# Kernel tuning notes

Measured on AMD Instinct MI355X. Metric: run time of the kernel, lower is better.

The kernel has to match this reference:

```python
import jax, jax.numpy as jnp
import numpy as np

LN_EPS = 1e-5  # torch nn.LayerNorm default


def _layernorm(h):
    # elementwise_affine=False LayerNorm over last dim
    mu = jnp.mean(h, axis=-1, keepdims=True)
    var = jnp.var(h, axis=-1, keepdims=True)
    return (h - mu) * jax.lax.rsqrt(var + LN_EPS)


def setup_inputs() -> dict:
    key = jax.random.key(0)
    ks = jax.random.split(key, 7)
    B, M, D, L = 10240, 8, 512, 3  # b=1024*10 and m=8 are hardcoded in the module
    rn = lambda k, shape, scale=1.0: jax.random.normal(k, shape, dtype=jnp.float32) * scale
    return {
        "x":   rn(ks[0], (B, D)),
        "Ws":  rn(ks[1], (L, M, D, D), 0.05),  # per-layer basis weight tensors (m,i,j)
        "bs":  rn(ks[2], (L, M, D), 0.05),     # per-layer basis biases (m,i)
        "pWs": rn(ks[3], (L, B, M)),           # per-sample weight-mixing coeffs
        "pbs": rn(ks[4], (L, B, M)),           # per-sample bias-mixing coeffs
        "gWs": rn(ks[5], (L, B, D, 1)),        # gates (squeezed in forward)
        "gbs": rn(ks[6], (L, B, D)),
    }


def reference(x, Ws, bs, pWs, pbs, gWs, gbs):
    L = Ws.shape[0]
    for l in range(L):
        gW = gWs[l][..., 0]                                  # (b, i)
        # 'bi,bm,mij,bj->bi' without materializing (b,i,j):
        y = jnp.einsum('mij,bj->bmi', Ws[l], x)              # (b, m, i)
        Wx = gW * jnp.einsum('bm,bmi->bi', pWs[l], y)        # (b, i)
        # 'bj,bm,mj->bj' (bias lives in output dim)
        bias = gbs[l] * jnp.einsum('bm,mi->bi', pbs[l], bs[l])
        h = Wx + bias
        if l != L - 1:  # hidden layers: LayerNorm (no affine) + ELU; last: identity
            h = jax.nn.elu(_layernorm(h))
        x = h
    return x
```

## Files before the change

kernel.cpp:

```cpp
#include <hip/hip_runtime.h>
#include <math.h>

#define BB   10240
#define DD   512
#define MM   8

typedef _Float16 h8 __attribute__((ext_vector_type(8)));
typedef float    f4 __attribute__((ext_vector_type(4)));

__device__ __forceinline__ void gload16(const void* g, void* l) {
    __builtin_amdgcn_global_load_lds(
        (__attribute__((address_space(1))) void*)(g),
        (__attribute__((address_space(3))) void*)(l), 16, 0, 0);
}

__global__ void __launch_bounds__(256) cvt_f32_f16(const float* __restrict__ s,
                                                   _Float16* __restrict__ d, int n8) {
    int i = blockIdx.x * 256 + threadIdx.x;
    if (i >= n8) return;
    const float4* sp = (const float4*)s + (size_t)i * 2;
    float4 a = sp[0], b = sp[1];
    h8 o = { (_Float16)a.x, (_Float16)a.y, (_Float16)a.z, (_Float16)a.w,
             (_Float16)b.x, (_Float16)b.y, (_Float16)b.z, (_Float16)b.w };
    *(h8*)(d + (size_t)i * 8) = o;
}

template <int HALF_OUT>
__global__ void __launch_bounds__(128, 2) gemm_layer(
    const _Float16* __restrict__ xh,
    const _Float16* __restrict__ Wh,
    const float*  __restrict__ pW,
    const float*  __restrict__ pb,
    const float*  __restrict__ bsv,
    const float*  __restrict__ gW,
    const float*  __restrict__ gb,
    float* __restrict__ outf,
    _Float16* __restrict__ outh)
{
    __shared__ __align__(16) _Float16 Wl[2][3][32 * 64];
    __shared__ __align__(16) _Float16 Ab[128 * 64];

    const int tid  = threadIdx.x;
    const int lane = tid & 63;
    const int w    = tid >> 6;
    const int ln16 = lane & 15, quad = lane >> 4;
    const int bn0  = blockIdx.x * 64;
    const int bm0  = blockIdx.y * 128;

    _Float16 pwh[8][8];
    #pragma unroll
    for (int mt = 0; mt < 8; ++mt) {
        const float* pp = pW + (size_t)(bm0 + mt * 16 + ln16) * MM;
        float4 p0 = *(const float4*)pp;
        float4 p1 = *(const float4*)(pp + 4);
        pwh[mt][0] = (_Float16)p0.x; pwh[mt][1] = (_Float16)p0.y;
        pwh[mt][2] = (_Float16)p0.z; pwh[mt][3] = (_Float16)p0.w;
        pwh[mt][4] = (_Float16)p1.x; pwh[mt][5] = (_Float16)p1.y;
        pwh[mt][6] = (_Float16)p1.z; pwh[mt][7] = (_Float16)p1.w;
    }

    f4 acc[8][2] = {};
    h8 afr[2][8];

#define STW(S_, M_, JC_) do {                                                  \
    _Pragma("unroll")                                                          \
    for (int c = 0; c < 4; ++c) {                                              \
        int rit     = c * 8 + (lane >> 3);                                     \
        int logical = (lane & 7) ^ (lane >> 3);                                \
        const _Float16* gp = Wh + (size_t)(M_) * (DD * DD)                     \
                               + (size_t)(bn0 + w * 32 + rit) * DD             \
                               + (JC_) * 64 + logical * 8;                     \
        gload16(gp, &Wl[w][S_][c * 512]);                                      \
    }                                                                          \
} while (0)

#define STA(JC_) do {                                                          \
    _Pragma("unroll")                                                          \
    for (int c = 0; c < 8; ++c) {                                              \
        int rit     = w * 64 + c * 8 + (lane >> 3);                            \
        int logical = (lane & 7) ^ (lane >> 3);                                \
        const _Float16* gp = xh + (size_t)(bm0 + rit) * DD                     \
                                + (JC_) * 64 + logical * 8;                    \
        gload16(gp, &Ab[rit * 64]);                                            \
    }                                                                          \
} while (0)

#define AFR() do {                                                             \
    _Pragma("unroll")                                                          \
    for (int _ks = 0; _ks < 2; ++_ks)                                          \
        _Pragma("unroll")                                                      \
        for (int _mt = 0; _mt < 8; ++_mt) {                                    \
            int _phys = (_ks * 4 + quad) ^ (ln16 & 7);                         \
            afr[_ks][_mt] = *(const h8*)&Ab[(_mt * 16 + ln16) * 64             \
                                            + _phys * 8];                      \
        }                                                                      \
} while (0)

#define GS(T_, N_, AF_, SA_, B1_, B2_) do {                                    \
    if ((T_) + 2 <= 63) STW((((T_) + 2) % 3), (((T_) + 2) & 7),                \
                            (((T_) + 2) >> 3));                                \
    asm volatile("s_waitcnt vmcnt(%0)" :: "i"(N_) : "memory");                 \
    __builtin_amdgcn_sched_barrier(0);                                         \
    if (AF_) AFR();                                                            \
    h8 wfr[2][2];                                                              \
    _Pragma("unroll")                                                          \
    for (int ks = 0; ks < 2; ++ks)                                             \
        _Pragma("unroll")                                                      \
        for (int nt = 0; nt < 2; ++nt) {                                       \
            int row  = nt * 16 + ln16;                                         \
            int phys = (ks * 4 + quad) ^ (ln16 & 7);                           \
            wfr[ks][nt] = *(const h8*)&Wl[w][(T_) % 3][row * 64 + phys * 8];   \
        }                                                                      \
    _Pragma("unroll")                                                          \
    for (int ks = 0; ks < 2; ++ks)                                             \
        _Pragma("unroll")                                                      \
        for (int mt = 0; mt < 8; ++mt) {                                       \
            h8 as = afr[ks][mt] * pwh[mt][(T_) & 7];      \
            acc[mt][0] = __builtin_amdgcn_mfma_f32_16x16x32_f16(               \
                as, wfr[ks][0], acc[mt][0], 0, 0, 0);                          \
            acc[mt][1] = __builtin_amdgcn_mfma_f32_16x16x32_f16(               \
                as, wfr[ks][1], acc[mt][1], 0, 0, 0);                          \
        }                                                                      \
    if (SA_) STA(((T_) >> 3) + 1);                                             \
    if (B2_) { asm volatile("s_waitcnt lgkmcnt(0)" ::: "memory");              \
               __builtin_amdgcn_s_barrier();                                   \
               asm volatile("" ::: "memory"); }                                \
    if (B1_) { __builtin_amdgcn_s_barrier();                                   \
               asm volatile("" ::: "memory"); }                                \
} while (0)

    STA(0);
    STW(0, 0, 0);
    STW(1, 1, 0);
    asm volatile("s_waitcnt vmcnt(8)" ::: "memory");
    __builtin_amdgcn_sched_barrier(0);
    __builtin_amdgcn_s_barrier();
    asm volatile("" ::: "memory");

    GS(  0,  8, 1, 0, 0, 1);
    GS(  1,  8, 0, 0, 0, 0);
    GS(  2,  8, 0, 1, 0, 0);
    GS(  3, 16, 0, 0, 0, 0);
    GS(  4, 16, 0, 0, 0, 0);
    GS(  5,  8, 0, 0, 0, 0);
    GS(  6,  8, 0, 0, 0, 0);
    GS(  7,  8, 0, 0, 1, 0);
    GS(  8,  8, 1, 0, 0, 1);
    GS(  9,  8, 0, 0, 0, 0);
    GS( 10,  8, 0, 1, 0, 0);
    GS( 11, 16, 0, 0, 0, 0);
    GS( 12, 16, 0, 0, 0, 0);
    GS( 13,  8, 0, 0, 0, 0);
    GS( 14,  8, 0, 0, 0, 0);
    GS( 15,  8, 0, 0, 1, 0);
    GS( 16,  8, 1, 0, 0, 1);
    GS( 17,  8, 0, 0, 0, 0);
    GS( 18,  8, 0, 1, 0, 0);
    GS( 19, 16, 0, 0, 0, 0);
    GS( 20, 16, 0, 0, 0, 0);
    GS( 21,  8, 0, 0, 0, 0);
    GS( 22,  8, 0, 0, 0, 0);
    GS( 23,  8, 0, 0, 1, 0);
    GS( 24,  8, 1, 0, 0, 1);
    GS( 25,  8, 0, 0, 0, 0);
    GS( 26,  8, 0, 1, 0, 0);
    GS( 27, 16, 0, 0, 0, 0);
    GS( 28, 16, 0, 0, 0, 0);
    GS( 29,  8, 0, 0, 0, 0);
    GS( 30,  8, 0, 0, 0, 0);
    GS( 31,  8, 0, 0, 1, 0);
    GS( 32,  8, 1, 0, 0, 1);
    GS( 33,  8, 0, 0, 0, 0);
    GS( 34,  8, 0, 1, 0, 0);
    GS( 35, 16, 0, 0, 0, 0);
    GS( 36, 16, 0, 0, 0, 0);
    GS( 37,  8, 0, 0, 0, 0);
    GS( 38,  8, 0, 0, 0, 0);
    GS( 39,  8, 0, 0, 1, 0);
    GS( 40,  8, 1, 0, 0, 1);
    GS( 41,  8, 0, 0, 0, 0);
    GS( 42,  8, 0, 1, 0, 0);
    GS( 43, 16, 0, 0, 0, 0);
    GS( 44, 16, 0, 0, 0, 0);
    GS( 45,  8, 0, 0, 0, 0);
    GS( 46,  8, 0, 0, 0, 0);
    GS( 47,  8, 0, 0, 1, 0);
    GS( 48,  8, 1, 0, 0, 1);
    GS( 49,  8, 0, 0, 0, 0);
    GS( 50,  8, 0, 1, 0, 0);
    GS( 51, 16, 0, 0, 0, 0);
    GS( 52, 16, 0, 0, 0, 0);
    GS( 53,  8, 0, 0, 0, 0);
    GS( 54,  8, 0, 0, 0, 0);
    GS( 55,  8, 0, 0, 1, 0);
    GS( 56,  8, 1, 0, 0, 0);
    GS( 57,  8, 0, 0, 0, 0);
    GS( 58,  8, 0, 0, 0, 0);
    GS( 59,  8, 0, 0, 0, 0);
    GS( 60,  8, 0, 0, 0, 0);
    GS( 61,  8, 0, 0, 0, 0);
    GS( 62,  4, 0, 0, 0, 0);
    GS( 63,  0, 0, 0, 0, 0);

#undef GS
#undef AFR
#undef STA
#undef STW

    const int i0 = bn0 + w * 32 + ln16;
    const int i1 = i0 + 16;
    float bs0[8], bs1[8];
    #pragma unroll
    for (int m2 = 0; m2 < 8; ++m2) {
        bs0[m2] = bsv[m2 * DD + i0];
        bs1[m2] = bsv[m2 * DD + i1];
    }
    #pragma unroll
    for (int mt = 0; mt < 8; ++mt) {
        #pragma unroll
        for (int r = 0; r < 4; ++r) {
            int b = bm0 + mt * 16 + quad * 4 + r;
            float4 p0 = *(const float4*)(pb + (size_t)b * MM);
            float4 p1 = *(const float4*)(pb + (size_t)b * MM + 4);
            float bias0 = p0.x*bs0[0] + p0.y*bs0[1] + p0.z*bs0[2] + p0.w*bs0[3]
                        + p1.x*bs0[4] + p1.y*bs0[5] + p1.z*bs0[6] + p1.w*bs0[7];
            float bias1 = p0.x*bs1[0] + p0.y*bs1[1] + p0.z*bs1[2] + p0.w*bs1[3]
                        + p1.x*bs1[4] + p1.y*bs1[5] + p1.z*bs1[6] + p1.w*bs1[7];
            float v0 = gW[(size_t)b * DD + i0] * acc[mt][0][r] + gb[(size_t)b * DD + i0] * bias0;
            float v1 = gW[(size_t)b * DD + i1] * acc[mt][1][r] + gb[(size_t)b * DD + i1] * bias1;
            if (HALF_OUT) {
                outh[(size_t)b * DD + i0] = (_Float16)v0;
                outh[(size_t)b * DD + i1] = (_Float16)v1;
            } else {
                outf[(size_t)b * DD + i0] = v0;
                outf[(size_t)b * DD + i1] = v1;
            }
        }
    }
}

__global__ void __launch_bounds__(256) ln_elu_h(const _Float16* __restrict__ h,
                                                _Float16* __restrict__ xo) {
    const int w    = threadIdx.x >> 6;
    const int lane = threadIdx.x & 63;
    const int row  = blockIdx.x * 4 + w;
    h8 v = *(const h8*)(h + (size_t)row * DD + lane * 8);
    float f[8], s = 0.f, q = 0.f;
    #pragma unroll
    for (int i = 0; i < 8; ++i) { f[i] = (float)v[i]; s += f[i]; q += f[i] * f[i]; }
    #pragma unroll
    for (int off = 1; off < 64; off <<= 1) {
        s += __shfl_xor(s, off);
        q += __shfl_xor(q, off);
    }
    float mu   = s * (1.0f / 512.0f);
    float var  = q * (1.0f / 512.0f) - mu * mu;
    float rstd = rsqrtf(var + 1e-5f);
    h8 o;
    #pragma unroll
    for (int i = 0; i < 8; ++i) {
        float t = (f[i] - mu) * rstd;
        t = t > 0.0f ? t : expm1f(t);
        o[i] = (_Float16)t;
    }
    *(h8*)(xo + (size_t)row * DD + lane * 8) = o;
}

extern "C" void kernel_launch(void* const* d_in, const int* in_sizes, int n_in,
                              void* d_out, int out_size, void* d_ws, size_t ws_size,
                              hipStream_t stream) {
    const float* x   = (const float*)d_in[0];
    const float* Ws  = (const float*)d_in[1];
    const float* bs  = (const float*)d_in[2];
    const float* pWs = (const float*)d_in[3];
    const float* pbs = (const float*)d_in[4];
    const float* gWs = (const float*)d_in[5];
    const float* gbs = (const float*)d_in[6];
    float* out = (float*)d_out;

    _Float16* Wh = (_Float16*)d_ws;
    _Float16* xh = Wh + (size_t)3 * MM * DD * DD;
    _Float16* hh = xh + (size_t)BB * DD;

    const int wsl = MM * DD * DD;
    const int bsl = MM * DD;
    const int pl  = BB * MM;
    const int gl  = BB * DD;

    cvt_f32_f16<<<3072, 256, 0, stream>>>(Ws, Wh, 786432);
    cvt_f32_f16<<<2560, 256, 0, stream>>>(x, xh, 655360);

    dim3 gg(DD / 64, BB / 128);

    gemm_layer<1><<<gg, 128, 0, stream>>>(xh, Wh, pWs, pbs, bs, gWs, gbs,
                                          nullptr, hh);
    ln_elu_h<<<BB / 4, 256, 0, stream>>>(hh, xh);
    gemm_layer<1><<<gg, 128, 0, stream>>>(xh, Wh + wsl, pWs + pl, pbs + pl,
                                          bs + bsl, gWs + gl, gbs + gl,
                                          nullptr, hh);
    ln_elu_h<<<BB / 4, 256, 0, stream>>>(hh, xh);
    gemm_layer<0><<<gg, 128, 0, stream>>>(xh, Wh + 2 * wsl, pWs + 2 * pl,
                                          pbs + 2 * pl, bs + 2 * bsl,
                                          gWs + 2 * gl, gbs + 2 * gl,
                                          out, nullptr);
}
```

Before: 361.2 us.

## Shrink GEMM tile to 64 rows, deepen W pipeline, prefetch B fragments, fuse converts

Halves the batch tile of the layer GEMM from 128 to 64 rows, doubling the grid and raising launch bounds to 3 blocks per CU. The weight staging ring goes from 3 to 4 stages, and LDS-to-register weight fragments are double-buffered one step ahead. The A-tile load is issued earlier in each step. The two fp32-to-fp16 conversion kernels are merged into one launch. Each B tile is reused across fewer rows, so more weight traffic per FLOP is traded for better occupancy and latency hiding.

```diff
diff --git a/kernel.cpp b/kernel.cpp
--- a/kernel.cpp
+++ b/kernel.cpp
@@ -14,19 +14,26 @@
         (__attribute__((address_space(3))) void*)(l), 16, 0, 0);
 }
 
-__global__ void __launch_bounds__(256) cvt_f32_f16(const float* __restrict__ s,
-                                                   _Float16* __restrict__ d, int n8) {
+#define N8_WS 786432
+#define N8_X  655360
+__global__ void __launch_bounds__(256) cvt_all(const float* __restrict__ Ws,
+                                               const float* __restrict__ x,
+                                               _Float16* __restrict__ Wh,
+                                               _Float16* __restrict__ xh) {
     int i = blockIdx.x * 256 + threadIdx.x;
-    if (i >= n8) return;
-    const float4* sp = (const float4*)s + (size_t)i * 2;
+    const float* s; _Float16* d; int idx;
+    if (i < N8_WS)            { s = Ws; d = Wh; idx = i; }
+    else if (i < N8_WS + N8_X){ s = x;  d = xh; idx = i - N8_WS; }
+    else return;
+    const float4* sp = (const float4*)s + (size_t)idx * 2;
     float4 a = sp[0], b = sp[1];
     h8 o = { (_Float16)a.x, (_Float16)a.y, (_Float16)a.z, (_Float16)a.w,
              (_Float16)b.x, (_Float16)b.y, (_Float16)b.z, (_Float16)b.w };
-    *(h8*)(d + (size_t)i * 8) = o;
+    *(h8*)(d + (size_t)idx * 8) = o;
 }
 
 template <int HALF_OUT>
-__global__ void __launch_bounds__(128, 2) gemm_layer(
+__global__ void __launch_bounds__(128, 3) gemm_layer(
     const _Float16* __restrict__ xh,
     const _Float16* __restrict__ Wh,
     const float*  __restrict__ pW,
@@ -37,19 +44,19 @@
     float* __restrict__ outf,
     _Float16* __restrict__ outh)
 {
-    __shared__ __align__(16) _Float16 Wl[2][3][32 * 64];
-    __shared__ __align__(16) _Float16 Ab[128 * 64];
+    __shared__ __align__(16) _Float16 Wl[2][4][32 * 64];
+    __shared__ __align__(16) _Float16 Ab[64 * 64];
 
     const int tid  = threadIdx.x;
     const int lane = tid & 63;
     const int w    = tid >> 6;
     const int ln16 = lane & 15, quad = lane >> 4;
     const int bn0  = blockIdx.x * 64;
-    const int bm0  = blockIdx.y * 128;
-
-    _Float16 pwh[8][8];
-    #pragma unroll
-    for (int mt = 0; mt < 8; ++mt) {
+    const int bm0  = blockIdx.y * 64;
+
+    _Float16 pwh[4][8];
+    #pragma unroll
+    for (int mt = 0; mt < 4; ++mt) {
         const float* pp = pW + (size_t)(bm0 + mt * 16 + ln16) * MM;
         float4 p0 = *(const float4*)pp;
         float4 p1 = *(const float4*)(pp + 4);
@@ -59,8 +66,9 @@
         pwh[mt][6] = (_Float16)p1.z; pwh[mt][7] = (_Float16)p1.w;
     }
 
-    f4 acc[8][2] = {};
-    h8 afr[2][8];
+    f4 acc[4][2] = {};
+    h8 afr[2][4];
+    h8 wfr[2][2][2];
 
 #define STW(S_, M_, JC_) do {                                                  \
     _Pragma("unroll")                                                          \
@@ -76,12 +84,12 @@
 
 #define STA(JC_) do {                                                          \
     _Pragma("unroll")                                                          \
-    for (int c = 0; c < 8; ++c) {                                              \
-        int rit     = w * 64 + c * 8 + (lane >> 3);                            \
+    for (int c = 0; c < 4; ++c) {                                              \
+        int rit     = w * 32 + c * 8 + (lane >> 3);                            \
         int logical = (lane & 7) ^ (lane >> 3);                                \
         const _Float16* gp = xh + (size_t)(bm0 + rit) * DD                     \
                                 + (JC_) * 64 + logical * 8;                    \
-        gload16(gp, &Ab[rit * 64]);                                            \
+        gload16(gp, &Ab[(w * 32 + c * 8) * 64]);                               \
     }                                                                          \
 } while (0)
 
@@ -89,7 +97,7 @@
     _Pragma("unroll")                                                          \
     for (int _ks = 0; _ks < 2; ++_ks)                                          \
         _Pragma("unroll")                                                      \
-        for (int _mt = 0; _mt < 8; ++_mt) {                                    \
+        for (int _mt = 0; _mt < 4; ++_mt) {                                    \
             int _phys = (_ks * 4 + quad) ^ (ln16 & 7);                         \
             afr[_ks][_mt] = *(const h8*)&Ab[(_mt * 16 + ln16) * 64             \
                                             + _phys * 8];                      \
@@ -97,31 +105,33 @@
 } while (0)
 
 #define GS(T_, N_, AF_, SA_, B1_, B2_) do {                                    \
-    if ((T_) + 2 <= 63) STW((((T_) + 2) % 3), (((T_) + 2) & 7),                \
-                            (((T_) + 2) >> 3));                                \
+    if ((T_) + 3 <= 63) STW((((T_) + 3) & 3), (((T_) + 3) & 7),                \
+                            (((T_) + 3) >> 3));                                \
+    if (SA_) STA(((T_) >> 3) + 1);                                             \
     asm volatile("s_waitcnt vmcnt(%0)" :: "i"(N_) : "memory");                 \
     __builtin_amdgcn_sched_barrier(0);                                         \
     if (AF_) AFR();                                                            \
-    h8 wfr[2][2];                                                              \
+    if ((T_) < 63) {                                                           \
+        _Pragma("unroll")                                                      \
+        for (int ks = 0; ks < 2; ++ks)                                         \
+            _Pragma("unroll")                                                  \
+            for (int nt = 0; nt < 2; ++nt) {                                   \
+                int row  = nt * 16 + ln16;                                     \
+                int phys = (ks * 4 + quad) ^ (ln16 & 7);                       \
+                wfr[((T_) + 1) & 1][ks][nt] =                                  \
+                    *(const h8*)&Wl[w][((T_) + 1) & 3][row * 64 + phys * 8];   \
+            }                                                                  \
+    }                                                                          \
     _Pragma("unroll")                                                          \
     for (int ks = 0; ks < 2; ++ks)                                             \
         _Pragma("unroll")                                                      \
-        for (int nt = 0; nt < 2; ++nt) {                                       \
-            int row  = nt * 16 + ln16;                                         \
-            int phys = (ks * 4 + quad) ^ (ln16 & 7);                           \
-            wfr[ks][nt] = *(const h8*)&Wl[w][(T_) % 3][row * 64 + phys * 8];   \
-        }                                                                      \
-    _Pragma("unroll")                                                          \
-    for (int ks = 0; ks < 2; ++ks)                                             \
-        _Pragma("unroll")                                                      \
-        for (int mt = 0; mt < 8; ++mt) {                                       \
+        for (int mt = 0; mt < 4; ++mt) {                                       \
             h8 as = afr[ks][mt] * pwh[mt][(T_) & 7];      \
             acc[mt][0] = __builtin_amdgcn_mfma_f32_16x16x32_f16(               \
-                as, wfr[ks][0], acc[mt][0], 0, 0, 0);                          \
+                as, wfr[(T_) & 1][ks][0], acc[mt][0], 0, 0, 0);                \
             acc[mt][1] = __builtin_amdgcn_mfma_f32_16x16x32_f16(               \
-                as, wfr[ks][1], acc[mt][1], 0, 0, 0);                          \
+                as, wfr[(T_) & 1][ks][1], acc[mt][1], 0, 0, 0);                \
         }                                                                      \
-    if (SA_) STA(((T_) >> 3) + 1);                                             \
     if (B2_) { asm volatile("s_waitcnt lgkmcnt(0)" ::: "memory");              \
                __builtin_amdgcn_s_barrier();                                   \
                asm volatile("" ::: "memory"); }                                \
@@ -132,64 +142,73 @@
     STA(0);
     STW(0, 0, 0);
     STW(1, 1, 0);
+    STW(2, 2, 0);
     asm volatile("s_waitcnt vmcnt(8)" ::: "memory");
     __builtin_amdgcn_sched_barrier(0);
+    #pragma unroll
+    for (int ks = 0; ks < 2; ++ks)
+        #pragma unroll
+        for (int nt = 0; nt < 2; ++nt) {
+            int row  = nt * 16 + ln16;
+            int phys = (ks * 4 + quad) ^ (ln16 & 7);
+            wfr[0][ks][nt] = *(const h8*)&Wl[w][0][row * 64 + phys * 8];
+        }
     __builtin_amdgcn_s_barrier();
     asm volatile("" ::: "memory");
 
     GS(  0,  8, 1, 0, 0, 1);
     GS(  1,  8, 0, 0, 0, 0);
-    GS(  2,  8, 0, 1, 0, 0);
-    GS(  3, 16, 0, 0, 0, 0);
-    GS(  4, 16, 0, 0, 0, 0);
+    GS(  2, 12, 0, 1, 0, 0);
+    GS(  3, 12, 0, 0, 0, 0);
+    GS(  4, 12, 0, 0, 0, 0);
     GS(  5,  8, 0, 0, 0, 0);
     GS(  6,  8, 0, 0, 0, 0);
     GS(  7,  8, 0, 0, 1, 0);
     GS(  8,  8, 1, 0, 0, 1);
     GS(  9,  8, 0, 0, 0, 0);
-    GS( 10,  8, 0, 1, 0, 0);
-    GS( 11, 16, 0, 0, 0, 0);
-    GS( 12, 16, 0, 0, 0, 0);
+    GS( 10, 12, 0, 1, 0, 0);
+    GS( 11, 12, 0, 0, 0, 0);
+    GS( 12, 12, 0, 0, 0, 0);
     GS( 13,  8, 0, 0, 0, 0);
     GS( 14,  8, 0, 0, 0, 0);
     GS( 15,  8, 0, 0, 1, 0);
     GS( 16,  8, 1, 0, 0, 1);
     GS( 17,  8, 0, 0, 0, 0);
-    GS( 18,  8, 0, 1, 0, 0);
-    GS( 19, 16, 0, 0, 0, 0);
-    GS( 20, 16, 0, 0, 0, 0);
+    GS( 18, 12, 0, 1, 0, 0);
+    GS( 19, 12, 0, 0, 0, 0);
+    GS( 20, 12, 0, 0, 0, 0);
     GS( 21,  8, 0, 0, 0, 0);
     GS( 22,  8, 0, 0, 0, 0);
     GS( 23,  8, 0, 0, 1, 0);
     GS( 24,  8, 1, 0, 0, 1);
     GS( 25,  8, 0, 0, 0, 0);
-    GS( 26,  8, 0, 1, 0, 0);
-    GS( 27, 16, 0, 0, 0, 0);
-    GS( 28, 16, 0, 0, 0, 0);
+    GS( 26, 12, 0, 1, 0, 0);
+    GS( 27, 12, 0, 0, 0, 0);
+    GS( 28, 12, 0, 0, 0, 0);
     GS( 29,  8, 0, 0, 0, 0);
     GS( 30,  8, 0, 0, 0, 0);
     GS( 31,  8, 0, 0, 1, 0);
     GS( 32,  8, 1, 0, 0, 1);
     GS( 33,  8, 0, 0, 0, 0);
-    GS( 34,  8, 0, 1, 0, 0);
-    GS( 35, 16, 0, 0, 0, 0);
-    GS( 36, 16, 0, 0, 0, 0);
+    GS( 34, 12, 0, 1, 0, 0);
+    GS( 35, 12, 0, 0, 0, 0);
+    GS( 36, 12, 0, 0, 0, 0);
     GS( 37,  8, 0, 0, 0, 0);
     GS( 38,  8, 0, 0, 0, 0);
     GS( 39,  8, 0, 0, 1, 0);
     GS( 40,  8, 1, 0, 0, 1);
     GS( 41,  8, 0, 0, 0, 0);
-    GS( 42,  8, 0, 1, 0, 0);
-    GS( 43, 16, 0, 0, 0, 0);
-    GS( 44, 16, 0, 0, 0, 0);
+    GS( 42, 12, 0, 1, 0, 0);
+    GS( 43, 12, 0, 0, 0, 0);
+    GS( 44, 12, 0, 0, 0, 0);
     GS( 45,  8, 0, 0, 0, 0);
     GS( 46,  8, 0, 0, 0, 0);
     GS( 47,  8, 0, 0, 1, 0);
     GS( 48,  8, 1, 0, 0, 1);
     GS( 49,  8, 0, 0, 0, 0);
-    GS( 50,  8, 0, 1, 0, 0);
-    GS( 51, 16, 0, 0, 0, 0);
-    GS( 52, 16, 0, 0, 0, 0);
+    GS( 50, 12, 0, 1, 0, 0);
+    GS( 51, 12, 0, 0, 0, 0);
+    GS( 52, 12, 0, 0, 0, 0);
     GS( 53,  8, 0, 0, 0, 0);
     GS( 54,  8, 0, 0, 0, 0);
     GS( 55,  8, 0, 0, 1, 0);
@@ -198,8 +217,8 @@
     GS( 58,  8, 0, 0, 0, 0);
     GS( 59,  8, 0, 0, 0, 0);
     GS( 60,  8, 0, 0, 0, 0);
-    GS( 61,  8, 0, 0, 0, 0);
-    GS( 62,  4, 0, 0, 0, 0);
+    GS( 61,  4, 0, 0, 0, 0);
+    GS( 62,  0, 0, 0, 0, 0);
     GS( 63,  0, 0, 0, 0, 0);
 
 #undef GS
@@ -216,7 +235,7 @@
         bs1[m2] = bsv[m2 * DD + i1];
     }
     #pragma unroll
-    for (int mt = 0; mt < 8; ++mt) {
+    for (int mt = 0; mt < 4; ++mt) {
         #pragma unroll
         for (int r = 0; r < 4; ++r) {
             int b = bm0 + mt * 16 + quad * 4 + r;
@@ -287,10 +306,9 @@
     const int pl  = BB * MM;
     const int gl  = BB * DD;
 
-    cvt_f32_f16<<<3072, 256, 0, stream>>>(Ws, Wh, 786432);
-    cvt_f32_f16<<<2560, 256, 0, stream>>>(x, xh, 655360);
-
-    dim3 gg(DD / 64, BB / 128);
+    cvt_all<<<(N8_WS + N8_X) / 256, 256, 0, stream>>>(Ws, x, Wh, xh);
+
+    dim3 gg(DD / 64, BB / 64);
 
     gemm_layer<1><<<gg, 128, 0, stream>>>(xh, Wh, pWs, pbs, bs, gWs, gbs,
                                           nullptr, hh);
```

Result: faster. 352.0 us (-2.6%).
